# Performance work log

Measured on AMD Instinct MI355X. Metric: run time of the kernel, lower is better.

## Reference

```python
import jax, jax.numpy as jnp
import numpy as np

N = 50000        # nodes
E = 300000       # edges
D_IN = 256
D_H = 256
D_OUT = 64       # num classes
L = 3            # num GAT layers
G = 500          # num graphs in batch
NEG_SLOPE = 0.2


def setup_inputs() -> dict:
    key = jax.random.key(0)
    ks = jax.random.split(key, 12)
    x = jax.random.normal(ks[0], (N, D_IN), dtype=jnp.float32)
    edge_index = jax.random.randint(ks[1], (2, E), 0, N, dtype=jnp.int64)
    batch = jnp.sort(jax.random.randint(ks[2], (N,), 0, G, dtype=jnp.int64))
    # GAT layer params (all layers same width since D_IN == D_H)
    Ws = jax.random.normal(ks[3], (L, D_H, D_H), dtype=jnp.float32) * 0.05
    atts = jax.random.normal(ks[4], (L, 2 * D_H, 1), dtype=jnp.float32) * 0.05
    bs = jnp.zeros((L, D_H), dtype=jnp.float32)
    # post_mp: Linear(D_H,D_H) -> Dropout(0) -> Linear(D_H,D_OUT)
    pW1 = jax.random.normal(ks[5], (D_H, D_H), dtype=jnp.float32) * 0.05
    pb1 = jnp.zeros((D_H,), dtype=jnp.float32)
    pW2 = jax.random.normal(ks[6], (D_OUT, D_H), dtype=jnp.float32) * 0.05
    pb2 = jnp.zeros((D_OUT,), dtype=jnp.float32)
    return dict(x=x, edge_index=edge_index, batch=batch, Ws=Ws, atts=atts,
                bs=bs, pW1=pW1, pb1=pb1, pW2=pW2, pb2=pb2)


def _gat_layer(x, W, att, b, src, dst):
    h = x @ W.T                                   # [N, D_H] (lin, no bias)
    xi = h[dst]                                   # target features  [E, D_H]
    xj = h[src]                                   # source features  [E, D_H]
    e = jnp.concatenate([xi, xj], axis=1) @ att   # [E, 1]
    e = jax.nn.leaky_relu(e[:, 0], NEG_SLOPE)     # [E]
    # segment softmax keyed by destination node
    m = jax.ops.segment_max(e, dst, num_segments=N)
    m = jnp.where(jnp.isfinite(m), m, 0.0)        # empty segments -> 0
    ee = jnp.exp(e - m[dst])
    s = jax.ops.segment_sum(ee, dst, num_segments=N)
    alpha = ee / (s[dst] + 1e-16)                 # [E]
    # weighted scatter-add aggregation (aggr='add'); heads=1, concat view is identity
    out = jax.ops.segment_sum(alpha[:, None] * xj, dst, num_segments=N)
    return out + b


def reference(x, edge_index, batch, Ws, atts, bs, pW1, pb1, pW2, pb2):
    src = edge_index[0]
    dst = edge_index[1]
    for l in range(L):
        x = _gat_layer(x, Ws[l], atts[l], bs[l], src, dst)
    # Dropout(p=0) is identity
    x = jax.nn.relu(x)
    g = jax.ops.segment_max(x, batch, num_segments=G)   # global_max_pool [G, D_H]
    h = g @ pW1.T + pb1
    out = h @ pW2.T + pb2
    return jax.nn.log_softmax(out, axis=1)
```

## Files before the change

kernel.cpp:

```cpp
#include <hip/hip_runtime.h>
#include <math.h>

#define NEG_SLOPE 0.2f

typedef __attribute__((ext_vector_type(8))) short s16x8;
typedef __attribute__((ext_vector_type(4))) float f32x4;
typedef unsigned short ushort_t;

__device__ inline ushort_t f2bf(float f) {
    unsigned u = __float_as_uint(f);
    unsigned r = (u + 0x7fff + ((u >> 16) & 1)) >> 16;
    return (ushort_t)r;
}
__device__ inline float bf2f(ushort_t u) {
    return __uint_as_float(((unsigned)u) << 16);
}

__global__ __launch_bounds__(256) void cvt_kernel(const float* __restrict__ in,
        ushort_t* __restrict__ out, int n4) {
    int i = blockIdx.x * 256 + threadIdx.x;
    if (i < n4) {
        float4 v = ((const float4*)in)[i];
        ushort4 o;
        o.x = f2bf(v.x); o.y = f2bf(v.y); o.z = f2bf(v.z); o.w = f2bf(v.w);
        ((ushort4*)out)[i] = o;
    }
}

__global__ void deg_kernel(const int* __restrict__ ei, int* __restrict__ deg, int E) {
    int e = blockIdx.x * blockDim.x + threadIdx.x;
    if (e < E) atomicAdd(&deg[ei[E + e]], 1);
}

__global__ __launch_bounds__(1024) void scan1(const int* __restrict__ deg,
        int* __restrict__ tscan, int* __restrict__ bsum, int n) {
    __shared__ int ws[16];
    int t = threadIdx.x;
    int gi = blockIdx.x * 1024 + t;
    int v = (gi < n) ? deg[gi] : 0;
    int lane = t & 63, w = t >> 6;
    int s = v;
#pragma unroll
    for (int off = 1; off < 64; off <<= 1) {
        int u = __shfl_up(s, off);
        if (lane >= off) s += u;
    }
    if (lane == 63) ws[w] = s;
    __syncthreads();
    if (w == 0) {
        int x = (lane < 16) ? ws[lane] : 0;
#pragma unroll
        for (int off = 1; off < 16; off <<= 1) {
            int u = __shfl_up(x, off);
            if (lane >= off) x += u;
        }
        if (lane < 16) ws[lane] = x;
    }
    __syncthreads();
    int woff = (w > 0) ? ws[w - 1] : 0;
    if (gi < n) tscan[gi] = woff + s - v;
    if (t == 1023) bsum[blockIdx.x] = woff + s;
}

__global__ void scan2(const int* __restrict__ bsum, int* __restrict__ boff,
                      int nb, int* __restrict__ total_out) {
    int lane = threadIdx.x;
    int v = (lane < nb) ? bsum[lane] : 0;
    int s = v;
#pragma unroll
    for (int off = 1; off < 64; off <<= 1) {
        int u = __shfl_up(s, off);
        if (lane >= off) s += u;
    }
    if (lane < nb) boff[lane] = s - v;
    if (lane == 63) *total_out = s;
}

__global__ __launch_bounds__(1024) void scan3(const int* __restrict__ tscan,
        const int* __restrict__ boff, int* __restrict__ rowptr,
        int* __restrict__ cursor, int n) {
    int i = blockIdx.x * 1024 + threadIdx.x;
    if (i < n) {
        int v = tscan[i] + boff[blockIdx.x];
        rowptr[i] = v;
        cursor[i] = v;
    }
}

__global__ void scatter_kernel(const int* __restrict__ ei, int* __restrict__ cursor,
                               int* __restrict__ adj, int E) {
    int e = blockIdx.x * blockDim.x + threadIdx.x;
    if (e < E) {
        int d = ei[E + e];
        int pos = atomicAdd(&cursor[d], 1);
        adj[pos] = ei[e];
    }
}

__global__ __launch_bounds__(256) void gemm_bf16(const ushort_t* __restrict__ A,
        const ushort_t* __restrict__ B, ushort_t* __restrict__ C) {
    __shared__ ushort_t As[128 * 32];
    __shared__ ushort_t Bs[128 * 32];
    const int t = threadIdx.x;
    const int lane = t & 63, wid = t >> 6;
    const int wr = wid >> 1, wc = wid & 1;
    const long brow = (long)blockIdx.x * 128;
    const int bcol = blockIdx.y * 128;

    f32x4 acc[4][4] = {};

    const int r0 = wid * 16 + (lane >> 2);
    const int kof = (lane & 3) * 8;
    const int fr = lane & 15, kg = lane >> 4;

    for (int kt = 0; kt < 256; kt += 32) {
        __builtin_amdgcn_global_load_lds(
            (const __attribute__((address_space(1))) void*)(A + (brow + r0) * 256 + kt + kof),
            (__attribute__((address_space(3))) void*)(As + wid * 512 + lane * 8), 16, 0, 0);
        __builtin_amdgcn_global_load_lds(
            (const __attribute__((address_space(1))) void*)(A + (brow + r0 + 64) * 256 + kt + kof),
            (__attribute__((address_space(3))) void*)(As + (wid + 4) * 512 + lane * 8), 16, 0, 0);
        __builtin_amdgcn_global_load_lds(
            (const __attribute__((address_space(1))) void*)(B + (bcol + r0) * 256 + kt + kof),
            (__attribute__((address_space(3))) void*)(Bs + wid * 512 + lane * 8), 16, 0, 0);
        __builtin_amdgcn_global_load_lds(
            (const __attribute__((address_space(1))) void*)(B + (bcol + r0 + 64) * 256 + kt + kof),
            (__attribute__((address_space(3))) void*)(Bs + (wid + 4) * 512 + lane * 8), 16, 0, 0);
        asm volatile("s_waitcnt vmcnt(0)" ::: "memory");
        __syncthreads();

        s16x8 a[4], b[4];
#pragma unroll
        for (int m = 0; m < 4; m++)
            a[m] = *(const s16x8*)(As + (wr * 64 + m * 16 + fr) * 32 + kg * 8);
#pragma unroll
        for (int nn = 0; nn < 4; nn++)
            b[nn] = *(const s16x8*)(Bs + (wc * 64 + nn * 16 + fr) * 32 + kg * 8);
#pragma unroll
        for (int m = 0; m < 4; m++)
#pragma unroll
            for (int nn = 0; nn < 4; nn++)
                acc[m][nn] = __builtin_amdgcn_mfma_f32_16x16x32_bf16(a[m], b[nn], acc[m][nn], 0, 0, 0);
        __syncthreads();
    }

    const int rg = lane >> 4;
#pragma unroll
    for (int m = 0; m < 4; m++) {
        long rbase = brow + wr * 64 + m * 16 + rg * 4;
#pragma unroll
        for (int nn = 0; nn < 4; nn++) {
            int col = bcol + wc * 64 + nn * 16 + fr;
#pragma unroll
            for (int r = 0; r < 4; r++)
                C[(rbase + r) * 256 + col] = f2bf(acc[m][nn][r]);
        }
    }
}

__global__ __launch_bounds__(256) void node_att(const ushort_t* __restrict__ H,
        const float* __restrict__ att, float* __restrict__ a_dst,
        float* __restrict__ a_src, int n) {
    int w = threadIdx.x >> 6, lane = threadIdx.x & 63;
    int node = blockIdx.x * 4 + w;
    if (node >= n) return;
    ushort4 h4 = *(const ushort4*)(H + (size_t)node * 256 + lane * 4);
    float4 aL = *(const float4*)(att + lane * 4);
    float4 aH = *(const float4*)(att + 256 + lane * 4);
    float hx = bf2f(h4.x), hy = bf2f(h4.y), hz = bf2f(h4.z), hw = bf2f(h4.w);
    float ai = hx * aL.x + hy * aL.y + hz * aL.z + hw * aL.w;
    float aj = hx * aH.x + hy * aH.y + hz * aH.z + hw * aH.w;
#pragma unroll
    for (int off = 32; off; off >>= 1) {
        ai += __shfl_xor(ai, off);
        aj += __shfl_xor(aj, off);
    }
    if (lane == 0) { a_dst[node] = ai; a_src[node] = aj; }
}

__global__ __launch_bounds__(256) void gat_agg(const ushort_t* __restrict__ H,
        const float* __restrict__ a_dst, const float* __restrict__ a_src,
        const int* __restrict__ rowptr, const int* __restrict__ adj,
        const float* __restrict__ bias, float* __restrict__ OUT,
        ushort_t* __restrict__ OUTbf, int n, int write_f32) {
    int w = threadIdx.x >> 6, lane = threadIdx.x & 63;
    int node = blockIdx.x * 4 + w;
    if (node >= n) return;
    int beg = rowptr[node], end = rowptr[node + 1];
    float ai = a_dst[node];

    float m = -3.4e38f;
    for (int j = beg + lane; j < end; j += 64) {
        float e = ai + a_src[adj[j]];
        e = (e > 0.f) ? e : NEG_SLOPE * e;
        m = fmaxf(m, e);
    }
#pragma unroll
    for (int off = 32; off; off >>= 1) m = fmaxf(m, __shfl_xor(m, off));

    float ssum = 0.f;
    float4 acc = make_float4(0.f, 0.f, 0.f, 0.f);
    for (int j0 = beg; j0 < end; j0 += 64) {
        int cnt = min(64, end - j0);
        int sidx = 0;
        float e = 0.f;
        if (lane < cnt) {
            sidx = adj[j0 + lane];
            float tt = ai + a_src[sidx];
            e = (tt > 0.f) ? tt : NEG_SLOPE * tt;
        }
        for (int j = 0; j < cnt; j++) {
            float ej = __shfl(e, j);
            int sj = __shfl(sidx, j);
            float wgt = expf(ej - m);
            ssum += wgt;
            ushort4 hv = *(const ushort4*)(H + (size_t)sj * 256 + lane * 4);
            acc.x = fmaf(wgt, bf2f(hv.x), acc.x);
            acc.y = fmaf(wgt, bf2f(hv.y), acc.y);
            acc.z = fmaf(wgt, bf2f(hv.z), acc.z);
            acc.w = fmaf(wgt, bf2f(hv.w), acc.w);
        }
    }
    float inv = 1.f / (ssum + 1e-16f);
    float4 b4 = *(const float4*)(bias + lane * 4);
    float4 o;
    o.x = acc.x * inv + b4.x;
    o.y = acc.y * inv + b4.y;
    o.z = acc.z * inv + b4.z;
    o.w = acc.w * inv + b4.w;
    if (write_f32)
        *(float4*)(OUT + (size_t)node * 256 + lane * 4) = o;
    ushort4 ub;
    ub.x = f2bf(o.x); ub.y = f2bf(o.y); ub.z = f2bf(o.z); ub.w = f2bf(o.w);
    *(ushort4*)(OUTbf + (size_t)node * 256 + lane * 4) = ub;
}

__global__ __launch_bounds__(1024) void pool_kernel(const float* __restrict__ X,
        const int* __restrict__ batch, float* __restrict__ gbuf, int n) {
    __shared__ float red[4][256];
    int g = blockIdx.x;
    int c = threadIdx.x & 255;
    int rg = threadIdx.x >> 8;
    int lo = 0, hi = n;
    while (lo < hi) { int mid = (lo + hi) >> 1; if (batch[mid] < g) lo = mid + 1; else hi = mid; }
    int start = lo;
    hi = n;
    while (lo < hi) { int mid = (lo + hi) >> 1; if (batch[mid] < g + 1) lo = mid + 1; else hi = mid; }
    int end_ = lo;
    float m = 0.f;
    for (int i = start + rg; i < end_; i += 4)
        m = fmaxf(m, X[(size_t)i * 256 + c]);
    red[rg][c] = m;
    __syncthreads();
    if (rg == 0) {
        m = fmaxf(fmaxf(red[0][c], red[1][c]), fmaxf(red[2][c], red[3][c]));
        gbuf[g * 256 + c] = m;
    }
}

__global__ __launch_bounds__(256) void final_kernel(const float* __restrict__ gbuf,
        const float* __restrict__ pW1, const float* __restrict__ pb1,
        const float* __restrict__ pW2, const float* __restrict__ pb2,
        float* __restrict__ out) {
    __shared__ float gl[256];
    __shared__ float h1[256];
    int g = blockIdx.x, t = threadIdx.x;
    gl[t] = gbuf[g * 256 + t];
    __syncthreads();
    float acc = pb1[t];
    for (int k = 0; k < 256; k++) acc = fmaf(gl[k], pW1[t * 256 + k], acc);
    h1[t] = acc;
    __syncthreads();
    if (t < 64) {
        float o = pb2[t];
        for (int k = 0; k < 256; k++) o = fmaf(h1[k], pW2[t * 256 + k], o);
        float mx = o;
#pragma unroll
        for (int off = 32; off; off >>= 1) mx = fmaxf(mx, __shfl_xor(mx, off));
        float ex = expf(o - mx);
        float s = ex;
#pragma unroll
        for (int off = 32; off; off >>= 1) s += __shfl_xor(s, off);
        out[g * 64 + t] = o - mx - logf(s);
    }
}

extern "C" void kernel_launch(void* const* d_in, const int* in_sizes, int n_in,
                              void* d_out, int out_size, void* d_ws, size_t ws_size,
                              hipStream_t stream) {
    const float* x     = (const float*)d_in[0];
    const int*   ei    = (const int*)d_in[1];
    const int*   batch = (const int*)d_in[2];
    const float* Ws    = (const float*)d_in[3];
    const float* atts  = (const float*)d_in[4];
    const float* bs    = (const float*)d_in[5];
    const float* pW1   = (const float*)d_in[6];
    const float* pb1   = (const float*)d_in[7];
    const float* pW2   = (const float*)d_in[8];
    const float* pb2   = (const float*)d_in[9];
    float* out = (float*)d_out;

    const int N = in_sizes[0] / 256;
    const int E = in_sizes[1] / 2;
    const int G = out_size / 64;
    const int L = in_sizes[3] / (256 * 256);
    const int MB = (N + 127) / 128;
    const int Npad = MB * 128;
    const int NT = (N + 1023) / 1024;

    char* ws = (char*)d_ws;
    size_t off = 0;
    auto alloc = [&](size_t bytes) -> char* {
        char* p = ws + off;
        off += (bytes + 255) & ~size_t(255);
        return p;
    };
    ushort_t* Hbf    = (ushort_t*)alloc((size_t)Npad * 256 * 2);
    float*    OUTf   = (float*)alloc((size_t)N * 256 * 4);
    ushort_t* Xbf    = (ushort_t*)alloc((size_t)Npad * 256 * 2);
    ushort_t* Wbf    = (ushort_t*)alloc((size_t)L * 256 * 256 * 2);
    float*    a_dst  = (float*)alloc((size_t)N * 4);
    float*    a_src  = (float*)alloc((size_t)N * 4);
    int*      deg    = (int*)alloc((size_t)N * 4);
    int*      rowptr = (int*)alloc((size_t)(N + 1) * 4);
    int*      cursor = (int*)alloc((size_t)N * 4);
    int*      adj    = (int*)alloc((size_t)E * 4);
    int*      tscan  = (int*)alloc((size_t)N * 4);
    int*      bsum   = (int*)alloc((size_t)64 * 4);
    int*      boff   = (int*)alloc((size_t)64 * 4);
    float*    gbuf   = (float*)alloc((size_t)G * 256 * 4);

    hipMemsetAsync(deg, 0, (size_t)N * 4, stream);
    int eb = (E + 255) / 256;
    deg_kernel<<<eb, 256, 0, stream>>>(ei, deg, E);
    scan1<<<NT, 1024, 0, stream>>>(deg, tscan, bsum, N);
    scan2<<<1, 64, 0, stream>>>(bsum, boff, NT, rowptr + N);
    scan3<<<NT, 1024, 0, stream>>>(tscan, boff, rowptr, cursor, N);
    scatter_kernel<<<eb, 256, 0, stream>>>(ei, cursor, adj, E);

    cvt_kernel<<<(N * 64 + 255) / 256, 256, 0, stream>>>(x, Xbf, N * 64);
    cvt_kernel<<<(L * 16384 + 255) / 256, 256, 0, stream>>>(Ws, Wbf, L * 16384);

    for (int l = 0; l < L; ++l) {
        dim3 ggrid(MB, 2);
        gemm_bf16<<<ggrid, 256, 0, stream>>>(Xbf, Wbf + (size_t)l * 65536, Hbf);
        node_att<<<(N + 3) / 4, 256, 0, stream>>>(Hbf, atts + (size_t)l * 512, a_dst, a_src, N);
        gat_agg<<<(N + 3) / 4, 256, 0, stream>>>(Hbf, a_dst, a_src, rowptr, adj,
                                                 bs + (size_t)l * 256, OUTf, Xbf, N,
                                                 (l == L - 1) ? 1 : 0);
    }
    pool_kernel<<<G, 1024, 0, stream>>>(OUTf, batch, gbuf, N);
    final_kernel<<<G, 256, 0, stream>>>(gbuf, pW1, pb1, pW2, pb2, out);
}
```

Baseline: 391.8 us.

## Fuse attention scores into GEMM epilogue, restructure aggregation, pool from bf16

Removes the separate node_att kernel. The GEMM epilogue now computes partial attention dot products and accumulates them into a_dst/a_src with atomics, after a per-layer memset. The aggregation kernel now processes 4 edges at a time per wave, with 16 lanes per edge loading 32-byte chunks, and reduces across groups with shuffles. This drops the per-edge shuffle-serialised loop and issues more memory loads in parallel. The fp32 output buffer is also removed and pooling reads bf16, which saves a write but lowers the precision of the final features.

```diff
diff --git a/kernel.cpp b/kernel.cpp
--- a/kernel.cpp
+++ b/kernel.cpp
@@ -6,6 +6,7 @@
 typedef __attribute__((ext_vector_type(8))) short s16x8;
 typedef __attribute__((ext_vector_type(4))) float f32x4;
 typedef unsigned short ushort_t;
+typedef unsigned int uint_t;
 
 __device__ inline ushort_t f2bf(float f) {
     unsigned u = __float_as_uint(f);
@@ -98,7 +99,9 @@
 }
 
 __global__ __launch_bounds__(256) void gemm_bf16(const ushort_t* __restrict__ A,
-        const ushort_t* __restrict__ B, ushort_t* __restrict__ C) {
+        const ushort_t* __restrict__ B, ushort_t* __restrict__ C,
+        const float* __restrict__ att, float* __restrict__ a_dst,
+        float* __restrict__ a_src, int n) {
     __shared__ ushort_t As[128 * 32];
     __shared__ ushort_t Bs[128 * 32];
     const int t = threadIdx.x;
@@ -145,44 +148,40 @@
     }
 
     const int rg = lane >> 4;
+    const float* attL = att;
+    const float* attR = att + 256;
 #pragma unroll
     for (int m = 0; m < 4; m++) {
         long rbase = brow + wr * 64 + m * 16 + rg * 4;
 #pragma unroll
-        for (int nn = 0; nn < 4; nn++) {
-            int col = bcol + wc * 64 + nn * 16 + fr;
-#pragma unroll
-            for (int r = 0; r < 4; r++)
-                C[(rbase + r) * 256 + col] = f2bf(acc[m][nn][r]);
+        for (int r = 0; r < 4; r++) {
+            long row = rbase + r;
+            float sL = 0.f, sR = 0.f;
+#pragma unroll
+            for (int nn = 0; nn < 4; nn++) {
+                int col = bcol + wc * 64 + nn * 16 + fr;
+                float v = acc[m][nn][r];
+                C[row * 256 + col] = f2bf(v);
+                sL = fmaf(v, attL[col], sL);
+                sR = fmaf(v, attR[col], sR);
+            }
+#pragma unroll
+            for (int off = 8; off; off >>= 1) {
+                sL += __shfl_xor(sL, off);
+                sR += __shfl_xor(sR, off);
+            }
+            if (fr == 0 && row < n) {
+                atomicAdd(&a_dst[row], sL);
+                atomicAdd(&a_src[row], sR);
+            }
         }
     }
-}
-
-__global__ __launch_bounds__(256) void node_att(const ushort_t* __restrict__ H,
-        const float* __restrict__ att, float* __restrict__ a_dst,
-        float* __restrict__ a_src, int n) {
-    int w = threadIdx.x >> 6, lane = threadIdx.x & 63;
-    int node = blockIdx.x * 4 + w;
-    if (node >= n) return;
-    ushort4 h4 = *(const ushort4*)(H + (size_t)node * 256 + lane * 4);
-    float4 aL = *(const float4*)(att + lane * 4);
-    float4 aH = *(const float4*)(att + 256 + lane * 4);
-    float hx = bf2f(h4.x), hy = bf2f(h4.y), hz = bf2f(h4.z), hw = bf2f(h4.w);
-    float ai = hx * aL.x + hy * aL.y + hz * aL.z + hw * aL.w;
-    float aj = hx * aH.x + hy * aH.y + hz * aH.z + hw * aH.w;
-#pragma unroll
-    for (int off = 32; off; off >>= 1) {
-        ai += __shfl_xor(ai, off);
-        aj += __shfl_xor(aj, off);
-    }
-    if (lane == 0) { a_dst[node] = ai; a_src[node] = aj; }
 }
 
 __global__ __launch_bounds__(256) void gat_agg(const ushort_t* __restrict__ H,
         const float* __restrict__ a_dst, const float* __restrict__ a_src,
         const int* __restrict__ rowptr, const int* __restrict__ adj,
-        const float* __restrict__ bias, float* __restrict__ OUT,
-        ushort_t* __restrict__ OUTbf, int n, int write_f32) {
+        const float* __restrict__ bias, ushort_t* __restrict__ OUTbf, int n) {
     int w = threadIdx.x >> 6, lane = threadIdx.x & 63;
     int node = blockIdx.x * 4 + w;
     if (node >= n) return;
@@ -198,44 +197,63 @@
 #pragma unroll
     for (int off = 32; off; off >>= 1) m = fmaxf(m, __shfl_xor(m, off));
 
+    const int g = lane >> 4, fl = lane & 15;
     float ssum = 0.f;
-    float4 acc = make_float4(0.f, 0.f, 0.f, 0.f);
-    for (int j0 = beg; j0 < end; j0 += 64) {
-        int cnt = min(64, end - j0);
-        int sidx = 0;
-        float e = 0.f;
-        if (lane < cnt) {
-            sidx = adj[j0 + lane];
+    float acc[16];
+#pragma unroll
+    for (int k = 0; k < 16; k++) acc[k] = 0.f;
+
+    for (int j0 = beg; j0 < end; j0 += 4) {
+        int j = j0 + g;
+        if (j < end) {
+            int sidx = adj[j];
             float tt = ai + a_src[sidx];
-            e = (tt > 0.f) ? tt : NEG_SLOPE * tt;
+            tt = (tt > 0.f) ? tt : NEG_SLOPE * tt;
+            float wgt = expf(tt - m);
+            ssum += wgt;
+            const ushort_t* hp = H + (size_t)sidx * 256 + fl * 16;
+            uint4 q0 = *(const uint4*)(hp);
+            uint4 q1 = *(const uint4*)(hp + 8);
+            uint_t qs[8] = {q0.x, q0.y, q0.z, q0.w, q1.x, q1.y, q1.z, q1.w};
+#pragma unroll
+            for (int k = 0; k < 8; k++) {
+                float flo = __uint_as_float(qs[k] << 16);
+                float fhi = __uint_as_float(qs[k] & 0xffff0000u);
+                acc[2 * k]     = fmaf(wgt, flo, acc[2 * k]);
+                acc[2 * k + 1] = fmaf(wgt, fhi, acc[2 * k + 1]);
+            }
         }
-        for (int j = 0; j < cnt; j++) {
-            float ej = __shfl(e, j);
-            int sj = __shfl(sidx, j);
-            float wgt = expf(ej - m);
-            ssum += wgt;
-            ushort4 hv = *(const ushort4*)(H + (size_t)sj * 256 + lane * 4);
-            acc.x = fmaf(wgt, bf2f(hv.x), acc.x);
-            acc.y = fmaf(wgt, bf2f(hv.y), acc.y);
-            acc.z = fmaf(wgt, bf2f(hv.z), acc.z);
-            acc.w = fmaf(wgt, bf2f(hv.w), acc.w);
+    }
+
+#pragma unroll
+    for (int k = 0; k < 16; k++) {
+        acc[k] += __shfl_xor(acc[k], 16);
+        acc[k] += __shfl_xor(acc[k], 32);
+    }
+    ssum += __shfl_xor(ssum, 16);
+    ssum += __shfl_xor(ssum, 32);
+
+    if (g == 0) {
+        float inv = 1.f / (ssum + 1e-16f);
+        float bv[16];
+        *(float4*)&bv[0]  = *(const float4*)(bias + fl * 16);
+        *(float4*)&bv[4]  = *(const float4*)(bias + fl * 16 + 4);
+        *(float4*)&bv[8]  = *(const float4*)(bias + fl * 16 + 8);
+        *(float4*)&bv[12] = *(const float4*)(bias + fl * 16 + 12);
+        uint_t ou[8];
+#pragma unroll
+        for (int k = 0; k < 8; k++) {
+            uint_t lo = f2bf(acc[2 * k] * inv + bv[2 * k]);
+            uint_t hi = f2bf(acc[2 * k + 1] * inv + bv[2 * k + 1]);
+            ou[k] = lo | (hi << 16);
         }
-    }
-    float inv = 1.f / (ssum + 1e-16f);
-    float4 b4 = *(const float4*)(bias + lane * 4);
-    float4 o;
-    o.x = acc.x * inv + b4.x;
-    o.y = acc.y * inv + b4.y;
-    o.z = acc.z * inv + b4.z;
-    o.w = acc.w * inv + b4.w;
-    if (write_f32)
-        *(float4*)(OUT + (size_t)node * 256 + lane * 4) = o;
-    ushort4 ub;
-    ub.x = f2bf(o.x); ub.y = f2bf(o.y); ub.z = f2bf(o.z); ub.w = f2bf(o.w);
-    *(ushort4*)(OUTbf + (size_t)node * 256 + lane * 4) = ub;
-}
-
-__global__ __launch_bounds__(1024) void pool_kernel(const float* __restrict__ X,
+        uint4* op = (uint4*)(OUTbf + (size_t)node * 256 + fl * 16);
+        op[0] = make_uint4(ou[0], ou[1], ou[2], ou[3]);
+        op[1] = make_uint4(ou[4], ou[5], ou[6], ou[7]);
+    }
+}
+
+__global__ __launch_bounds__(1024) void pool_kernel(const ushort_t* __restrict__ X,
         const int* __restrict__ batch, float* __restrict__ gbuf, int n) {
     __shared__ float red[4][256];
     int g = blockIdx.x;
@@ -249,7 +267,7 @@
     int end_ = lo;
     float m = 0.f;
     for (int i = start + rg; i < end_; i += 4)
-        m = fmaxf(m, X[(size_t)i * 256 + c]);
+        m = fmaxf(m, bf2f(X[(size_t)i * 256 + c]));
     red[rg][c] = m;
     __syncthreads();
     if (rg == 0) {
@@ -316,11 +334,11 @@
         return p;
     };
     ushort_t* Hbf    = (ushort_t*)alloc((size_t)Npad * 256 * 2);
-    float*    OUTf   = (float*)alloc((size_t)N * 256 * 4);
     ushort_t* Xbf    = (ushort_t*)alloc((size_t)Npad * 256 * 2);
     ushort_t* Wbf    = (ushort_t*)alloc((size_t)L * 256 * 256 * 2);
-    float*    a_dst  = (float*)alloc((size_t)N * 4);
-    float*    a_src  = (float*)alloc((size_t)N * 4);
+    float*    a_both = (float*)alloc((size_t)2 * N * 4);
+    float*    a_dst  = a_both;
+    float*    a_src  = a_both + N;
     int*      deg    = (int*)alloc((size_t)N * 4);
     int*      rowptr = (int*)alloc((size_t)(N + 1) * 4);
     int*      cursor = (int*)alloc((size_t)N * 4);
@@ -342,13 +360,13 @@
     cvt_kernel<<<(L * 16384 + 255) / 256, 256, 0, stream>>>(Ws, Wbf, L * 16384);
 
     for (int l = 0; l < L; ++l) {
+        hipMemsetAsync(a_both, 0, (size_t)2 * N * 4, stream);
         dim3 ggrid(MB, 2);
-        gemm_bf16<<<ggrid, 256, 0, stream>>>(Xbf, Wbf + (size_t)l * 65536, Hbf);
-        node_att<<<(N + 3) / 4, 256, 0, stream>>>(Hbf, atts + (size_t)l * 512, a_dst, a_src, N);
+        gemm_bf16<<<ggrid, 256, 0, stream>>>(Xbf, Wbf + (size_t)l * 65536, Hbf,
+                                             atts + (size_t)l * 512, a_dst, a_src, N);
         gat_agg<<<(N + 3) / 4, 256, 0, stream>>>(Hbf, a_dst, a_src, rowptr, adj,
-                                                 bs + (size_t)l * 256, OUTf, Xbf, N,
-                                                 (l == L - 1) ? 1 : 0);
-    }
-    pool_kernel<<<G, 1024, 0, stream>>>(OUTf, batch, gbuf, N);
+                                                 bs + (size_t)l * 256, Xbf, N);
+    }
+    pool_kernel<<<G, 1024, 0, stream>>>(Xbf, batch, gbuf, N);
     final_kernel<<<G, 256, 0, stream>>>(gbuf, pW1, pb1, pW2, pb2, out);
 }
```

New measurement: 368.3 us. 6.0% less time.
